# Performance work log

Measured on AMD Instinct MI355X. Metric: run time of the kernel, lower is better.

Reference implementation:

```python
import jax, jax.numpy as jnp
import numpy as np

B, T, V, E, H, DE = 64, 52, 10000, 512, 512, 2048


def _lstm_cell(x, h, c, w_ih, w_hh, b_ih, b_hh):
    # torch.nn.LSTMCell gate order: i, f, g, o
    gates = x @ w_ih.T + h @ w_hh.T + b_ih + b_hh
    i, f, g, o = jnp.split(gates, 4, axis=-1)
    c2 = jax.nn.sigmoid(f) * c + jax.nn.sigmoid(i) * jnp.tanh(g)
    h2 = jax.nn.sigmoid(o) * jnp.tanh(c2)
    return h2, c2


def _run_dir(emb_seq, img, lens, p1, p2, fc_w, fc_b):
    # emb_seq: [B, Td, E]; img: [B, H]; lens: [B] sorted descending.
    # The torch loop slices h[:batch_size_t]; since lens is sorted descending,
    # that is equivalent to masking updates where t >= (len-1). Rows that fall
    # out of the active prefix are never read again, and their predictions stay 0.
    Bd, Td = emb_seq.shape[0], emb_seq.shape[1]
    Hd = img.shape[1]
    mask = jnp.arange(Td)[None, :] < (lens - 1)[:, None]  # [B, Td]
    z = jnp.zeros((Bd, Hd), emb_seq.dtype)

    def step(carry, xs):
        h, c, h1, c1 = carry
        x, m = xs
        m2 = m[:, None]
        hn, cn = _lstm_cell(x, h, c, *p1)
        h1n, c1n = _lstm_cell(jnp.concatenate([hn, img], axis=1), h1, c1, *p2)
        carry = (jnp.where(m2, hn, h), jnp.where(m2, cn, c),
                 jnp.where(m2, h1n, h1), jnp.where(m2, c1n, c1))
        preds = jnp.where(m2, h1n @ fc_w.T + fc_b, 0.0)  # [B, V]
        return carry, preds

    _, preds = jax.lax.scan(step, (z, z, z, z), (emb_seq.transpose(1, 0, 2), mask.T))
    return preds.transpose(1, 0, 2)  # [B, Td, V]


def setup_inputs():
    key = jax.random.key(0)
    ks = iter(jax.random.split(key, 48))

    def u(shape, a=-0.1, b=0.1):
        return jax.random.uniform(next(ks), shape, minval=a, maxval=b, dtype=jnp.float32)

    inp = {}
    inp['encoder_out'] = jax.random.normal(next(ks), (B, DE), dtype=jnp.float32)
    inp['encoded_captions'] = jax.random.randint(next(ks), (B, T), 0, V)
    cl = jax.random.randint(next(ks), (B, 1), 2, T + 1)
    inp['caption_lengths'] = cl.at[0, 0].set(T)  # ensure max decode length = T-1
    # embeddings (uniform -0.1..0.1 per init_weights)
    inp['emb_w'] = u((V, E))
    inp['emb_r_w'] = u((V, E))
    # LSTM cells: torch default init uniform(-1/sqrt(H), 1/sqrt(H))
    kH = 1.0 / np.sqrt(H)
    for name, din in [('1', E), ('2', 2 * H), ('r1', E), ('r2', 2 * H)]:
        inp['w_ih' + name] = u((4 * H, din), -kH, kH)
        inp['w_hh' + name] = u((4 * H, H), -kH, kH)
        inp['b_ih' + name] = u((4 * H,), -kH, kH)
        inp['b_hh' + name] = u((4 * H,), -kH, kH)
    kD = 1.0 / np.sqrt(DE)
    inp['img_f_w'] = u((H, DE), -kD, kD)
    inp['img_f_b'] = u((H,), -kD, kD)
    inp['img_b_w'] = u((H, DE), -kD, kD)
    inp['img_b_b'] = u((H,), -kD, kD)
    inp['fc_w'] = u((V, H))
    inp['fc_b'] = jnp.zeros((V,), jnp.float32)
    inp['fcr_w'] = u((V, H))
    inp['fcr_b'] = jnp.zeros((V,), jnp.float32)
    return inp


def reference(encoder_out, encoded_captions, caption_lengths, emb_w, emb_r_w,
              w_ih1, w_hh1, b_ih1, b_hh1, w_ih2, w_hh2, b_ih2, b_hh2,
              w_ihr1, w_hhr1, b_ihr1, b_hhr1, w_ihr2, w_hhr2, b_ihr2, b_hhr2,
              img_f_w, img_f_b, img_b_w, img_b_b, fc_w, fc_b, fcr_w, fcr_b):
    lens = caption_lengths[:, 0]
    order = jnp.argsort(-lens)  # descending, stable (jax argsort is stable)
    lens = lens[order]
    enc = encoder_out[order]
    caps = encoded_captions[order]
    Tc = caps.shape[1]
    # per-row reversal of the first len tokens; rest zero (matches torch loop)
    j = jnp.arange(Tc)[None, :]
    valid = j < lens[:, None]
    rev_idx = jnp.where(valid, lens[:, None] - 1 - j, 0)
    caps_rev = jnp.where(valid, jnp.take_along_axis(caps, rev_idx, axis=1), 0)
    emb = emb_w[caps]          # [B, T, E]
    emb_r = emb_r_w[caps_rev]  # [B, T, E]
    img_f = enc @ img_f_w.T + img_f_b
    img_r = enc @ img_b_w.T + img_b_b
    Td = Tc - 1  # max(decode_lengths); setup guarantees max(lens) == T
    preds = _run_dir(emb[:, :Td], img_f, lens,
                     (w_ih1, w_hh1, b_ih1, b_hh1), (w_ih2, w_hh2, b_ih2, b_hh2), fc_w, fc_b)
    preds_r = _run_dir(emb_r[:, :Td], img_r, lens,
                       (w_ihr1, w_hhr1, b_ihr1, b_hhr1), (w_ihr2, w_hhr2, b_ihr2, b_hhr2), fcr_w, fcr_b)
    return preds, preds_r, caps, caps_rev, lens - 1, order
```

## Files before the change

kernel.cpp:

```cpp
#include <hip/hip_runtime.h>
#include <stdint.h>

#define B64   64
#define T52   52
#define TD    51
#define V10K  10000
#define MP    3328
#define MR    3264
#define NPFC  10112

typedef float  f32x4  __attribute__((ext_vector_type(4)));
typedef __bf16 bf16x8 __attribute__((ext_vector_type(8)));
typedef unsigned int u32x4 __attribute__((ext_vector_type(4)));
typedef unsigned short ushort_t;

__device__ inline unsigned short f2bf(float f) {
  unsigned u = __builtin_bit_cast(unsigned, f);
  u += 0x7fffu + ((u >> 16) & 1u);
  return (unsigned short)(u >> 16);
}
__device__ inline unsigned pack2(float a, float b) {
  return (unsigned)f2bf(a) | ((unsigned)f2bf(b) << 16);
}
__device__ inline float sigm(float x) { return 1.f / (1.f + expf(-x)); }

__device__ inline void store2_sc(ushort_t* p, unsigned v) {
  asm volatile("global_store_short %0, %1, off sc1" :: "v"(p), "v"(v) : "memory");
}

__global__ void k_prep(const int* __restrict__ cl, const int* __restrict__ caps,
                       float* __restrict__ out_caps, float* __restrict__ out_capr,
                       float* __restrict__ out_lm1, float* __restrict__ out_ord,
                       int* __restrict__ order_i, int* __restrict__ lensm1_i,
                       int* __restrict__ nvtab, int* __restrict__ capsS,
                       int* __restrict__ capsRev)
{
  __shared__ int L[64], O[64], Ls_s[64];
  int i = threadIdx.x;
  L[i] = cl[i];
  __syncthreads();
  if (i == 0) {
    for (int a = 0; a < 64; ++a) O[a] = a;
    for (int a = 1; a < 64; ++a) {
      int key = O[a], kl = L[key], b = a - 1;
      while (b >= 0 && L[O[b]] < kl) { O[b + 1] = O[b]; --b; }
      O[b + 1] = key;
    }
  }
  __syncthreads();
  int src = O[i];
  int Ls  = L[src];
  Ls_s[i] = Ls;
  order_i[i]  = src;
  lensm1_i[i] = Ls - 1;
  out_lm1[i]  = (float)(Ls - 1);
  out_ord[i]  = (float)src;
  int rowLocal[T52];
  for (int t = 0; t < T52; ++t) {
    int c = caps[src * T52 + t];
    rowLocal[t] = c;
    capsS[i * T52 + t]    = c;
    out_caps[i * T52 + t] = (float)c;
  }
  for (int j = 0; j < T52; ++j) {
    int rv = (j < Ls) ? rowLocal[Ls - 1 - j] : 0;
    capsRev[i * T52 + j]  = rv;
    out_capr[i * T52 + j] = (float)rv;
  }
  __syncthreads();
  if (i < TD) {
    int nv = 0;
    for (int r = 0; r < 64; ++r) nv += (Ls_s[r] - 1 > i) ? 1 : 0;
    nvtab[i] = nv;
  }
}

__global__ void k_convert(const float* __restrict__ w_ih1, const float* __restrict__ w_ihr1,
                          const float* __restrict__ fc_w, const float* __restrict__ fcr_w,
                          const float* __restrict__ b_ih1, const float* __restrict__ b_hh1,
                          const float* __restrict__ b_ihr1, const float* __restrict__ b_hhr1,
                          const float* __restrict__ w_hh1, const float* __restrict__ w_hhr1,
                          const float* __restrict__ w_ih2, const float* __restrict__ w_ihr2,
                          const float* __restrict__ w_hh2, const float* __restrict__ w_hhr2,
                          const float* __restrict__ img_f_w, const float* __restrict__ img_b_w,
                          const float* __restrict__ b_ih2, const float* __restrict__ b_hh2,
                          const float* __restrict__ b_ihr2, const float* __restrict__ b_hhr2,
                          const float* __restrict__ enc, const int* __restrict__ order_i,
                          ushort_t* __restrict__ wih1bf, ushort_t* __restrict__ fcwbf,
                          ushort_t* __restrict__ whh1bf, ushort_t* __restrict__ wih2Lbf,
                          ushort_t* __restrict__ whh2bf, ushort_t* __restrict__ wih2Ibf,
                          ushort_t* __restrict__ imgwbf, ushort_t* __restrict__ encbf,
                          float* __restrict__ biasg1, float* __restrict__ biasg2)
{
  long long gid = (long long)blockIdx.x * blockDim.x + threadIdx.x;
  const long long C1 = 2048LL * 512 / 8;
  const long long CF = (long long)NPFC * 512 / 8;
  const long long bs  = 2 * C1 + 2 * CF;
  const long long bs2 = bs + 6 * C1;
  const long long bs3 = bs2 + 2 * C1;
  const long long bs4 = bs3 + 2 * C1;
  const long long bs5 = bs4 + 32768;
  if (gid < 2 * C1) {
    int dir = gid >= C1; long long cid = gid - (long long)dir * C1;
    const float* s = (dir ? w_ihr1 : w_ih1) + cid * 8;
    ushort_t* d = wih1bf + (long long)dir * 2048 * 512 + cid * 8;
    uint4 v;
    v.x = pack2(s[0], s[1]); v.y = pack2(s[2], s[3]);
    v.z = pack2(s[4], s[5]); v.w = pack2(s[6], s[7]);
    *(uint4*)d = v;
  } else if (gid < bs) {
    long long g2 = gid - 2 * C1; int dir = g2 >= CF;
    long long cid = g2 - (long long)dir * CF;
    long long row = cid >> 6; int k8 = (int)(cid & 63) * 8;
    ushort_t* d = fcwbf + (long long)dir * NPFC * 512 + row * 512 + k8;
    uint4 v;
    if (row < V10K) {
      const float* s = (dir ? fcr_w : fc_w) + row * 512 + k8;
      v.x = pack2(s[0], s[1]); v.y = pack2(s[2], s[3]);
      v.z = pack2(s[4], s[5]); v.w = pack2(s[6], s[7]);
    } else { v.x = v.y = v.z = v.w = 0u; }
    *(uint4*)d = v;
  } else if (gid < bs2) {
    long long e = gid - bs;
    int arr = (int)(e / (2 * C1));
    long long d2 = e - (long long)arr * 2 * C1;
    int dir = d2 >= C1;
    long long cid = d2 - (long long)dir * C1;
    long long row = cid >> 6; int k8 = (int)(cid & 63) * 8;
    const float* s;
    ushort_t* d;
    if (arr == 0)      { s = (dir ? w_hhr1 : w_hh1) + row * 512  + k8; d = whh1bf; }
    else if (arr == 1) { s = (dir ? w_ihr2 : w_ih2) + row * 1024 + k8; d = wih2Lbf; }
    else               { s = (dir ? w_hhr2 : w_hh2) + row * 512  + k8; d = whh2bf; }
    d += (long long)dir * 2048 * 512 + cid * 8;
    uint4 v;
    v.x = pack2(s[0], s[1]); v.y = pack2(s[2], s[3]);
    v.z = pack2(s[4], s[5]); v.w = pack2(s[6], s[7]);
    *(uint4*)d = v;
  } else if (gid < bs3) {
    long long e = gid - bs2; int dir = e >= C1;
    long long cid = e - (long long)dir * C1;
    long long row = cid >> 6; int k8 = (int)(cid & 63) * 8;
    const float* s = (dir ? w_ihr2 : w_ih2) + row * 1024 + 512 + k8;
    ushort_t* d = wih2Ibf + (long long)dir * 2048 * 512 + cid * 8;
    uint4 v;
    v.x = pack2(s[0], s[1]); v.y = pack2(s[2], s[3]);
    v.z = pack2(s[4], s[5]); v.w = pack2(s[6], s[7]);
    *(uint4*)d = v;
  } else if (gid < bs4) {
    long long e = gid - bs3; int dir = e >= C1;
    long long cid = e - (long long)dir * C1;
    long long row = cid >> 8; int c8 = (int)(cid & 255) * 8;
    const float* s = (dir ? img_b_w : img_f_w) + row * 2048 + c8;
    ushort_t* d = imgwbf + (long long)dir * 512 * 2048 + cid * 8;
    uint4 v;
    v.x = pack2(s[0], s[1]); v.y = pack2(s[2], s[3]);
    v.z = pack2(s[4], s[5]); v.w = pack2(s[6], s[7]);
    *(uint4*)d = v;
  } else if (gid < bs5) {
    long long cid = gid - bs4;
    int m = (int)(cid >> 8); int c8 = (int)(cid & 255) * 8;
    const float* s = enc + (long long)order_i[m & 63] * 2048 + c8;
    ushort_t* d = encbf + cid * 8;
    uint4 v;
    v.x = pack2(s[0], s[1]); v.y = pack2(s[2], s[3]);
    v.z = pack2(s[4], s[5]); v.w = pack2(s[6], s[7]);
    *(uint4*)d = v;
  } else {
    long long g3 = gid - bs5;
    if (g3 < 4096) {
      int dir = g3 >= 2048; int j = (int)(g3 & 2047);
      biasg1[dir * 2048 + j] = dir ? (b_ihr1[j] + b_hhr1[j]) : (b_ih1[j] + b_hh1[j]);
    } else if (g3 < 8192) {
      long long g4 = g3 - 4096;
      int dir = g4 >= 2048; int j = (int)(g4 & 2047);
      biasg2[dir * 2048 + j] = dir ? (b_ihr2[j] + b_hhr2[j]) : (b_ih2[j] + b_hh2[j]);
    }
  }
}

__global__ void k_gather(const float* __restrict__ emb_w, const float* __restrict__ emb_r_w,
                         const int* __restrict__ capsS, const int* __restrict__ capsRev,
                         ushort_t* __restrict__ embA)
{
  long long gid = (long long)blockIdx.x * 256 + threadIdx.x;
  const long long CPD = (long long)MP * 512 / 8;
  if (gid >= 2 * CPD) return;
  int dir = gid >= CPD; long long cid = gid - (long long)dir * CPD;
  int m = (int)(cid >> 6); int k8 = (int)(cid & 63) * 8;
  ushort_t* d = embA + (long long)dir * MP * 512 + (long long)m * 512 + k8;
  uint4 v;
  if (m < MR) {
    int b = m / TD, t = m - b * TD;
    int row = dir ? capsRev[b * T52 + t] : capsS[b * T52 + t];
    const float* s = (dir ? emb_r_w : emb_w) + (long long)row * 512 + k8;
    v.x = pack2(s[0], s[1]); v.y = pack2(s[2], s[3]);
    v.z = pack2(s[4], s[5]); v.w = pack2(s[6], s[7]);
  } else { v.x = v.y = v.z = v.w = 0u; }
  *(uint4*)d = v;
}

template<int MODE>
__global__ __launch_bounds__(256)
void k_gemm(const ushort_t* __restrict__ A0, long long As,
            const ushort_t* __restrict__ B0, long long Bs,
            const float* __restrict__ bias0, const float* __restrict__ bias1,
            void* __restrict__ out0, long long Os,
            const int* __restrict__ lensm1, int Nreal, int K)
{
  __shared__ ushort_t Ab[128 * 32];
  __shared__ ushort_t Bb[128 * 32];
  int dirz = blockIdx.z;
  const ushort_t* A = A0 + dirz * As;
  const ushort_t* Bm = B0 + dirz * Bs;
  const float* bias = dirz ? bias1 : bias0;
  int tid = threadIdx.x;
  int lane = tid & 63, wid = tid >> 6;
  int wr = wid >> 1, wc = wid & 1;
  long long tm = (long long)blockIdx.x * 128, tn = (long long)blockIdx.y * 128;
  f32x4 acc[4][4] = {};
  int c0 = tid, c1 = tid + 256;
  const ushort_t* Ag0 = A + (tm + (c0 >> 2)) * K + (c0 & 3) * 8;
  const ushort_t* Ag1 = A + (tm + (c1 >> 2)) * K + (c1 & 3) * 8;
  const ushort_t* Bg0 = Bm + (tn + (c0 >> 2)) * K + (c0 & 3) * 8;
  const ushort_t* Bg1 = Bm + (tn + (c1 >> 2)) * K + (c1 & 3) * 8;
  int KK = K >> 5;
  for (int kk = 0; kk < KK; ++kk) {
    uint4 va0 = *(const uint4*)(Ag0 + kk * 32);
    uint4 va1 = *(const uint4*)(Ag1 + kk * 32);
    uint4 vb0 = *(const uint4*)(Bg0 + kk * 32);
    uint4 vb1 = *(const uint4*)(Bg1 + kk * 32);
    __syncthreads();
    *(uint4*)&Ab[c0 * 8] = va0;
    *(uint4*)&Ab[c1 * 8] = va1;
    *(uint4*)&Bb[c0 * 8] = vb0;
    *(uint4*)&Bb[c1 * 8] = vb1;
    __syncthreads();
    int koff = (lane >> 4) * 8;
    bf16x8 av[4], bv[4];
    #pragma unroll
    for (int mi = 0; mi < 4; ++mi)
      av[mi] = *(const bf16x8*)&Ab[(wr * 64 + mi * 16 + (lane & 15)) * 32 + koff];
    #pragma unroll
    for (int ni = 0; ni < 4; ++ni)
      bv[ni] = *(const bf16x8*)&Bb[(wc * 64 + ni * 16 + (lane & 15)) * 32 + koff];
    #pragma unroll
    for (int mi = 0; mi < 4; ++mi)
      #pragma unroll
      for (int ni = 0; ni < 4; ++ni)
        acc[mi][ni] = __builtin_amdgcn_mfma_f32_16x16x32_bf16(av[mi], bv[ni], acc[mi][ni], 0, 0, 0);
  }
  #pragma unroll
  for (int mi = 0; mi < 4; ++mi) {
    #pragma unroll
    for (int rr = 0; rr < 4; ++rr) {
      long long m = tm + wr * 64 + mi * 16 + ((lane >> 4) * 4) + rr;
      if (MODE == 0) {
        float* orow = (float*)out0 + dirz * Os + m * (long long)Nreal;
        #pragma unroll
        for (int ni = 0; ni < 4; ++ni) {
          int n = (int)tn + wc * 64 + ni * 16 + (lane & 15);
          orow[n] = acc[mi][ni][rr] + bias[n];
        }
      } else if (MODE == 1) {
        if (m < MR) {
          int bb = (int)(m / TD); int tt = (int)(m - (long long)bb * TD);
          bool valid = tt < lensm1[bb];
          float* orow = (float*)out0 + dirz * Os + m * (long long)Nreal;
          #pragma unroll
          for (int ni = 0; ni < 4; ++ni) {
            int n = (int)tn + wc * 64 + ni * 16 + (lane & 15);
            if (n < Nreal) orow[n] = valid ? (acc[mi][ni][rr] + bias[n]) : 0.f;
          }
        }
      } else if (MODE == 2) {
        float bm = bias[m];
        float* orow = (float*)out0 + dirz * Os + m * (long long)Nreal;
        #pragma unroll
        for (int ni = 0; ni < 4; ++ni) {
          int n = (int)tn + wc * 64 + ni * 16 + (lane & 15);
          if (n < Nreal) orow[n] = acc[mi][ni][rr] + bm;
        }
      } else {
        ushort_t* orow = (ushort_t*)out0 + dirz * Os + m * (long long)Nreal;
        #pragma unroll
        for (int ni = 0; ni < 4; ++ni) {
          int n = (int)tn + wc * 64 + ni * 16 + (lane & 15);
          orow[n] = f2bf(acc[mi][ni][rr] + bias[n]);
        }
      }
    }
  }
}

__global__ __launch_bounds__(128, 1)
void k_rec(const ushort_t* __restrict__ whh1bf, const ushort_t* __restrict__ wih2Lbf,
           const ushort_t* __restrict__ whh2bf, const float* __restrict__ xg1,
           const float* __restrict__ xg2imgT,
           ushort_t* __restrict__ h1hist,
           ushort_t* __restrict__ h2hist,
           ushort_t* __restrict__ h2allbf, const int* __restrict__ nvtab,
           int* __restrict__ slots)
{
  __builtin_amdgcn_fence(__ATOMIC_ACQUIRE, "agent");
  const int bid = blockIdx.x;
  const int grp = bid & 7;
  const int ht  = bid >> 3;
  const bool isL2 = grp >= 4;
  const int dir  = (grp >> 1) & 1;
  const int half = grp & 1;
  const int tid = threadIdx.x;
  const int lane = tid & 63, mt = tid >> 6;
  const int l15 = lane & 15, l4 = lane >> 4;
  const int jl = ht * 16 + l15;
  const int rbase = half * 32 + mt * 16;
  const int r0 = rbase + l4 * 4;

  __shared__ ushort_t Wl[32768];
  __shared__ ushort_t Wi[32768];
  __shared__ int nv_s[64];

  {
    const ushort_t* src = (isL2 ? whh2bf : whh1bf) + (long long)dir * 2048 * 512;
    #pragma unroll
    for (int i = 0; i < 32; ++i) {
      int c = tid + i * 128;
      int nl = c >> 6;
      int kb = (c & 63) * 16;
      int row = (nl >> 4) * 512 + ht * 16 + (nl & 15);
      u32x4 v = *(const u32x4*)(src + (long long)row * 512 + (long long)(c & 63) * 8);
      *(u32x4*)((char*)Wl + nl * 1024 + (kb ^ ((nl & 7) << 4))) = v;
    }
    if (isL2) {
      const ushort_t* src2 = wih2Lbf + (long long)dir * 2048 * 512;
      #pragma unroll
      for (int i = 0; i < 32; ++i) {
        int c = tid + i * 128;
        int nl = c >> 6;
        int kb = (c & 63) * 16;
        int row = (nl >> 4) * 512 + ht * 16 + (nl & 15);
        u32x4 v = *(const u32x4*)(src2 + (long long)row * 512 + (long long)(c & 63) * 8);
        *(u32x4*)((char*)Wi + nl * 1024 + (kb ^ ((nl & 7) << 4))) = v;
      }
    }
    if (tid < TD) nv_s[tid] = nvtab[tid];
  }
  __syncthreads();

  int* aS = slots + (dir * 2 + half) * 32;
  int* bS = slots + 128 + (dir * 2 + half) * 32;

  if (!isL2) {
    f32x4 creg = {0.f, 0.f, 0.f, 0.f};
    for (int t = 0; t < TD; ++t) {
      bool act = (rbase < nv_s[t]);
      float xs[4][4];
      if (act) {
        #pragma unroll
        for (int g = 0; g < 4; ++g)
          #pragma unroll
          for (int rr = 0; rr < 4; ++rr)
            xs[g][rr] = xg1[((long long)dir * MP + (long long)(r0 + rr) * TD + t) * 2048
                            + g * 512 + jl];
      }
      if (t > 0) {
        if (mt == 0) {
          for (;;) {
            int v = __hip_atomic_load(&aS[lane & 31], __ATOMIC_RELAXED, __HIP_MEMORY_SCOPE_AGENT);
            if (__all(v >= t)) break;
            __builtin_amdgcn_s_sleep(1);
          }
        }
        __syncthreads();
      }
      if (act) {
        const ushort_t* hsrc = h1hist + ((long long)t * 2 + dir) * (64 * 512)
                             + (long long)(rbase + l15) * 512 + l4 * 8;
        u32x4 hv[16];
        #pragma unroll
        for (int kk = 0; kk < 16; ++kk)
          hv[kk] = *(const u32x4*)(hsrc + kk * 32);
        f32x4 acc[4] = {};
        #pragma unroll
        for (int kk = 0; kk < 16; ++kk) {
          bf16x8 av = __builtin_bit_cast(bf16x8, hv[kk]);
          int kb = kk * 64 + l4 * 16;
          #pragma unroll
          for (int g = 0; g < 4; ++g) {
            bf16x8 bv = *(const bf16x8*)((const char*)Wl + (g * 16 + l15) * 1024 + (kb ^ ((l15 & 7) << 4)));
            acc[g] = __builtin_amdgcn_mfma_f32_16x16x32_bf16(av, bv, acc[g], 0, 0, 0);
          }
        }
        ushort_t* hdst = h1hist + ((long long)(t + 1) * 2 + dir) * (64 * 512);
        f32x4 cn;
        #pragma unroll
        for (int rr = 0; rr < 4; ++rr) {
          float gi = acc[0][rr] + xs[0][rr];
          float gf = acc[1][rr] + xs[1][rr];
          float gg = acc[2][rr] + xs[2][rr];
          float go = acc[3][rr] + xs[3][rr];
          float c = sigm(gf) * creg[rr] + sigm(gi) * tanhf(gg);
          float h = sigm(go) * tanhf(c);
          cn[rr] = c;
          store2_sc(hdst + (long long)(r0 + rr) * 512 + jl, (unsigned)f2bf(h));
        }
        creg = cn;
      }
      __syncthreads();
      if (tid == 0)
        __hip_atomic_store(&aS[ht], t + 1, __ATOMIC_RELAXED, __HIP_MEMORY_SCOPE_AGENT);
    }
  } else {
    f32x4 xv2[4];
    {
      const float* xg = xg2imgT + (long long)dir * (2048 * 64);
      #pragma unroll
      for (int g = 0; g < 4; ++g)
        xv2[g] = *(const f32x4*)(xg + (long long)(g * 512 + jl) * 64 + r0);
    }
    f32x4 creg = {0.f, 0.f, 0.f, 0.f};
    for (int t = 0; t < TD; ++t) {
      bool act = (rbase < nv_s[t]);
      int nv = nv_s[t];
      if (mt == 0) {
        for (;;) {
          int v = __hip_atomic_load(&aS[lane & 31], __ATOMIC_RELAXED, __HIP_MEMORY_SCOPE_AGENT);
          if (__all(v >= t + 1)) break;
          __builtin_amdgcn_s_sleep(1);
        }
      }
      __syncthreads();
      f32x4 acc[4] = {};
      if (act) {
        const ushort_t* h1s = h1hist + ((long long)(t + 1) * 2 + dir) * (64 * 512)
                            + (long long)(rbase + l15) * 512 + l4 * 8;
        u32x4 ha[16];
        #pragma unroll
        for (int kk = 0; kk < 16; ++kk) ha[kk] = *(const u32x4*)(h1s + kk * 32);
        #pragma unroll
        for (int kk = 0; kk < 16; ++kk) {
          bf16x8 av = __builtin_bit_cast(bf16x8, ha[kk]);
          int kb = kk * 64 + l4 * 16;
          #pragma unroll
          for (int g = 0; g < 4; ++g) {
            bf16x8 bv = *(const bf16x8*)((const char*)Wi + (g * 16 + l15) * 1024 + (kb ^ ((l15 & 7) << 4)));
            acc[g] = __builtin_amdgcn_mfma_f32_16x16x32_bf16(av, bv, acc[g], 0, 0, 0);
          }
        }
      }
      if (mt == 0) {
        for (;;) {
          int v = __hip_atomic_load(&bS[lane & 31], __ATOMIC_RELAXED, __HIP_MEMORY_SCOPE_AGENT);
          if (__all(v >= t)) break;
          __builtin_amdgcn_s_sleep(1);
        }
      }
      __syncthreads();
      if (act) {
        const ushort_t* h2s = h2hist + ((long long)t * 2 + dir) * (64 * 512)
                            + (long long)(rbase + l15) * 512 + l4 * 8;
        u32x4 hb[16];
        #pragma unroll
        for (int kk = 0; kk < 16; ++kk) hb[kk] = *(const u32x4*)(h2s + kk * 32);
        #pragma unroll
        for (int kk = 0; kk < 16; ++kk) {
          bf16x8 av = __builtin_bit_cast(bf16x8, hb[kk]);
          int kb = kk * 64 + l4 * 16;
          #pragma unroll
          for (int g = 0; g < 4; ++g) {
            bf16x8 bv = *(const bf16x8*)((const char*)Wl + (g * 16 + l15) * 1024 + (kb ^ ((l15 & 7) << 4)));
            acc[g] = __builtin_amdgcn_mfma_f32_16x16x32_bf16(av, bv, acc[g], 0, 0, 0);
          }
        }
        ushort_t* h2n = h2hist + ((long long)(t + 1) * 2 + dir) * (64 * 512);
        ushort_t* h2a = h2allbf + (long long)dir * MP * 512;
        f32x4 cn;
        #pragma unroll
        for (int rr = 0; rr < 4; ++rr) {
          float gi = acc[0][rr] + xv2[0][rr];
          float gf = acc[1][rr] + xv2[1][rr];
          float gg = acc[2][rr] + xv2[2][rr];
          float go = acc[3][rr] + xv2[3][rr];
          float c = sigm(gf) * creg[rr] + sigm(gi) * tanhf(gg);
          float h = sigm(go) * tanhf(c);
          cn[rr] = c;
          ushort_t hbb = f2bf(h);
          store2_sc(h2n + (long long)(r0 + rr) * 512 + jl, (unsigned)hbb);
          if (r0 + rr < nv)
            h2a[((long long)(r0 + rr) * TD + t) * 512 + jl] = hbb;
        }
        creg = cn;
      }
      __syncthreads();
      if (tid == 0)
        __hip_atomic_store(&bS[ht], t + 1, __ATOMIC_RELAXED, __HIP_MEMORY_SCOPE_AGENT);
    }
  }
}

extern "C" void kernel_launch(void* const* d_in, const int* in_sizes, int n_in,
                              void* d_out, int out_size, void* d_ws, size_t ws_size,
                              hipStream_t stream)
{
  const float* enc     = (const float*)d_in[0];
  const int*   caps    = (const int*)d_in[1];
  const int*   cl      = (const int*)d_in[2];
  const float* emb_w   = (const float*)d_in[3];
  const float* emb_r_w = (const float*)d_in[4];
  const float* w_ih1   = (const float*)d_in[5];
  const float* w_hh1   = (const float*)d_in[6];
  const float* b_ih1   = (const float*)d_in[7];
  const float* b_hh1   = (const float*)d_in[8];
  const float* w_ih2   = (const float*)d_in[9];
  const float* w_hh2   = (const float*)d_in[10];
  const float* b_ih2   = (const float*)d_in[11];
  const float* b_hh2   = (const float*)d_in[12];
  const float* w_ihr1  = (const float*)d_in[13];
  const float* w_hhr1  = (const float*)d_in[14];
  const float* b_ihr1  = (const float*)d_in[15];
  const float* b_hhr1  = (const float*)d_in[16];
  const float* w_ihr2  = (const float*)d_in[17];
  const float* w_hhr2  = (const float*)d_in[18];
  const float* b_ihr2  = (const float*)d_in[19];
  const float* b_hhr2  = (const float*)d_in[20];
  const float* img_f_w = (const float*)d_in[21];
  const float* img_f_b = (const float*)d_in[22];
  const float* img_b_w = (const float*)d_in[23];
  const float* img_b_b = (const float*)d_in[24];
  const float* fc_w    = (const float*)d_in[25];
  const float* fc_b    = (const float*)d_in[26];
  const float* fcr_w   = (const float*)d_in[27];
  const float* fcr_b   = (const float*)d_in[28];

  float* outF = (float*)d_out;
  const long long PRED = (long long)MR * V10K;
  float* o_caps = outF + 2 * PRED;
  float* o_capr = o_caps + B64 * T52;
  float* o_lm1  = o_capr + B64 * T52;
  float* o_ord  = o_lm1 + B64;
  float*    xg1       = outF;
  ushort_t* whh1bf    = (ushort_t*)(outF + 27500000);
  ushort_t* wih2Lbf   = (ushort_t*)(outF + 28600000);
  ushort_t* whh2bf    = (ushort_t*)(outF + 29700000);
  ushort_t* h1hist    = (ushort_t*)(outF + 31000000);
  ushort_t* h2hist    = (ushort_t*)(outF + 32800000);
  ushort_t* wih2Ibf   = (ushort_t*)(outF + 34600000);
  ushort_t* imgwbf    = (ushort_t*)(outF + 35700000);
  ushort_t* encbf     = (ushort_t*)(outF + 36800000);
  ushort_t* imgbf     = (ushort_t*)(outF + 37000000);

  char* w = (char*)d_ws;
  auto alloc = [&](size_t bytes) -> char* {
    char* p = w; w += (bytes + 255) & ~(size_t)255; return p;
  };
  int*      order_i  = (int*)alloc(64 * 4);
  int*      lensm1_i = (int*)alloc(64 * 4);
  int*      nvtab    = (int*)alloc(64 * 4);
  int*      capsS    = (int*)alloc(B64 * T52 * 4);
  int*      capsRev  = (int*)alloc(B64 * T52 * 4);
  float*    biasg1   = (float*)alloc(2 * 2048 * 4);
  float*    biasg2   = (float*)alloc(2 * 2048 * 4);
  float*    xg2imgT  = (float*)alloc((size_t)2 * 2048 * 64 * 4);
  int*      slotp    = (int*)alloc(1024);
  ushort_t* embA    = (ushort_t*)alloc((size_t)2 * MP * 512 * 2);
  ushort_t* wih1bf  = (ushort_t*)alloc((size_t)2 * 2048 * 512 * 2);
  ushort_t* fcwbf   = (ushort_t*)alloc((size_t)2 * NPFC * 512 * 2);
  ushort_t* h2allbf = (ushort_t*)alloc((size_t)2 * MP * 512 * 2);

  hipMemsetAsync(slotp, 0, 1024, stream);
  hipMemsetAsync(h1hist, 0, 131072, stream);
  hipMemsetAsync(h2hist, 0, 131072, stream);

  k_prep<<<1, 64, 0, stream>>>(cl, caps, o_caps, o_capr, o_lm1, o_ord,
                               order_i, lensm1_i, nvtab, capsS, capsRev);
  k_convert<<<11360, 256, 0, stream>>>(w_ih1, w_ihr1, fc_w, fcr_w,
                                       b_ih1, b_hh1, b_ihr1, b_hhr1,
                                       w_hh1, w_hhr1, w_ih2, w_ihr2, w_hh2, w_hhr2,
                                       img_f_w, img_b_w, b_ih2, b_hh2, b_ihr2, b_hhr2,
                                       enc, order_i,
                                       wih1bf, fcwbf, whh1bf, wih2Lbf, whh2bf,
                                       wih2Ibf, imgwbf, encbf, biasg1, biasg2);
  k_gather<<<1664, 256, 0, stream>>>(emb_w, emb_r_w, capsS, capsRev, embA);
  k_gemm<3><<<dim3(1, 4, 2), 256, 0, stream>>>(encbf, 0LL,
                                               imgwbf, 512LL * 2048,
                                               img_f_b, img_b_b,
                                               imgbf, 128LL * 512,
                                               nullptr, 512, 2048);
  k_gemm<2><<<dim3(16, 1, 2), 256, 0, stream>>>(wih2Ibf, 2048LL * 512,
                                                imgbf, 128LL * 512,
                                                biasg2, biasg2 + 2048,
                                                xg2imgT, 2048LL * 64,
                                                nullptr, 64, 512);
  k_gemm<0><<<dim3(26, 16, 2), 256, 0, stream>>>(embA, (long long)MP * 512,
                                                 wih1bf, 2048LL * 512,
                                                 biasg1, biasg1 + 2048,
                                                 xg1, (long long)MP * 2048,
                                                 nullptr, 2048, 512);
  k_rec<<<256, 128, 0, stream>>>(whh1bf, wih2Lbf, whh2bf, xg1, xg2imgT,
                                 h1hist, h2hist, h2allbf, nvtab, slotp);
  k_gemm<1><<<dim3(26, 79, 2), 256, 0, stream>>>(h2allbf, (long long)MP * 512,
                                                 fcwbf, (long long)NPFC * 512,
                                                 fc_b, fcr_b,
                                                 outF, PRED,
                                                 lensm1_i, V10K, 512);
}
```

Baseline: 843.5 us.

## Fuse FC projection into persistent recurrence kernel, overlapping output GEMM with time steps

Replaces the recurrence kernel plus the separate vocabulary-projection GEMM with one persistent kernel. 64 blocks run layer 1, 128 blocks run layer 2 with a double-buffered h2 state, and 64 blocks compute the FC output for each time step as soon as that step's h2 is published. The FC blocks also zero the inactive prediction rows while waiting. Input-gate activations for layer 1 are written straight into the predictions buffer and read back from there, and hidden-state loads use batched sc1 inline-asm loads. The goal is to hide the large FC GEMM behind the serial recurrence. The cost is a smaller, less efficient per-step FC tile and more spin-wait synchronisation.

```diff
diff --git a/kernel.cpp b/kernel.cpp
--- a/kernel.cpp
+++ b/kernel.cpp
@@ -26,6 +26,77 @@
 
 __device__ inline void store2_sc(ushort_t* p, unsigned v) {
   asm volatile("global_store_short %0, %1, off sc1" :: "v"(p), "v"(v) : "memory");
+}
+__device__ inline void loadA16(const ushort_t* a, u32x4 (&h)[16]) {
+  asm volatile(
+    "global_load_dwordx4 %0,  %16, off sc1\n\t"
+    "global_load_dwordx4 %1,  %16, off offset:64 sc1\n\t"
+    "global_load_dwordx4 %2,  %16, off offset:128 sc1\n\t"
+    "global_load_dwordx4 %3,  %16, off offset:192 sc1\n\t"
+    "global_load_dwordx4 %4,  %16, off offset:256 sc1\n\t"
+    "global_load_dwordx4 %5,  %16, off offset:320 sc1\n\t"
+    "global_load_dwordx4 %6,  %16, off offset:384 sc1\n\t"
+    "global_load_dwordx4 %7,  %16, off offset:448 sc1\n\t"
+    "global_load_dwordx4 %8,  %16, off offset:512 sc1\n\t"
+    "global_load_dwordx4 %9,  %16, off offset:576 sc1\n\t"
+    "global_load_dwordx4 %10, %16, off offset:640 sc1\n\t"
+    "global_load_dwordx4 %11, %16, off offset:704 sc1\n\t"
+    "global_load_dwordx4 %12, %16, off offset:768 sc1\n\t"
+    "global_load_dwordx4 %13, %16, off offset:832 sc1\n\t"
+    "global_load_dwordx4 %14, %16, off offset:896 sc1\n\t"
+    "global_load_dwordx4 %15, %16, off offset:960 sc1\n\t"
+    "s_waitcnt vmcnt(0)"
+    : "=&v"(h[0]),"=&v"(h[1]),"=&v"(h[2]),"=&v"(h[3]),
+      "=&v"(h[4]),"=&v"(h[5]),"=&v"(h[6]),"=&v"(h[7]),
+      "=&v"(h[8]),"=&v"(h[9]),"=&v"(h[10]),"=&v"(h[11]),
+      "=&v"(h[12]),"=&v"(h[13]),"=&v"(h[14]),"=&v"(h[15])
+    : "v"(a) : "memory");
+}
+__device__ inline void loadA32(const ushort_t* a, const ushort_t* b,
+                               u32x4 (&ha)[16], u32x4 (&hb)[16]) {
+  asm volatile(
+    "global_load_dwordx4 %0,  %32, off sc1\n\t"
+    "global_load_dwordx4 %1,  %32, off offset:64 sc1\n\t"
+    "global_load_dwordx4 %2,  %32, off offset:128 sc1\n\t"
+    "global_load_dwordx4 %3,  %32, off offset:192 sc1\n\t"
+    "global_load_dwordx4 %4,  %32, off offset:256 sc1\n\t"
+    "global_load_dwordx4 %5,  %32, off offset:320 sc1\n\t"
+    "global_load_dwordx4 %6,  %32, off offset:384 sc1\n\t"
+    "global_load_dwordx4 %7,  %32, off offset:448 sc1\n\t"
+    "global_load_dwordx4 %8,  %32, off offset:512 sc1\n\t"
+    "global_load_dwordx4 %9,  %32, off offset:576 sc1\n\t"
+    "global_load_dwordx4 %10, %32, off offset:640 sc1\n\t"
+    "global_load_dwordx4 %11, %32, off offset:704 sc1\n\t"
+    "global_load_dwordx4 %12, %32, off offset:768 sc1\n\t"
+    "global_load_dwordx4 %13, %32, off offset:832 sc1\n\t"
+    "global_load_dwordx4 %14, %32, off offset:896 sc1\n\t"
+    "global_load_dwordx4 %15, %32, off offset:960 sc1\n\t"
+    "global_load_dwordx4 %16, %33, off sc1\n\t"
+    "global_load_dwordx4 %17, %33, off offset:64 sc1\n\t"
+    "global_load_dwordx4 %18, %33, off offset:128 sc1\n\t"
+    "global_load_dwordx4 %19, %33, off offset:192 sc1\n\t"
+    "global_load_dwordx4 %20, %33, off offset:256 sc1\n\t"
+    "global_load_dwordx4 %21, %33, off offset:320 sc1\n\t"
+    "global_load_dwordx4 %22, %33, off offset:384 sc1\n\t"
+    "global_load_dwordx4 %23, %33, off offset:448 sc1\n\t"
+    "global_load_dwordx4 %24, %33, off offset:512 sc1\n\t"
+    "global_load_dwordx4 %25, %33, off offset:576 sc1\n\t"
+    "global_load_dwordx4 %26, %33, off offset:640 sc1\n\t"
+    "global_load_dwordx4 %27, %33, off offset:704 sc1\n\t"
+    "global_load_dwordx4 %28, %33, off offset:768 sc1\n\t"
+    "global_load_dwordx4 %29, %33, off offset:832 sc1\n\t"
+    "global_load_dwordx4 %30, %33, off offset:896 sc1\n\t"
+    "global_load_dwordx4 %31, %33, off offset:960 sc1\n\t"
+    "s_waitcnt vmcnt(0)"
+    : "=&v"(ha[0]),"=&v"(ha[1]),"=&v"(ha[2]),"=&v"(ha[3]),
+      "=&v"(ha[4]),"=&v"(ha[5]),"=&v"(ha[6]),"=&v"(ha[7]),
+      "=&v"(ha[8]),"=&v"(ha[9]),"=&v"(ha[10]),"=&v"(ha[11]),
+      "=&v"(ha[12]),"=&v"(ha[13]),"=&v"(ha[14]),"=&v"(ha[15]),
+      "=&v"(hb[0]),"=&v"(hb[1]),"=&v"(hb[2]),"=&v"(hb[3]),
+      "=&v"(hb[4]),"=&v"(hb[5]),"=&v"(hb[6]),"=&v"(hb[7]),
+      "=&v"(hb[8]),"=&v"(hb[9]),"=&v"(hb[10]),"=&v"(hb[11]),
+      "=&v"(hb[12]),"=&v"(hb[13]),"=&v"(hb[14]),"=&v"(hb[15])
+    : "v"(a), "v"(b) : "memory");
 }
 
 __global__ void k_prep(const int* __restrict__ cl, const int* __restrict__ caps,
@@ -206,7 +277,7 @@
             const ushort_t* __restrict__ B0, long long Bs,
             const float* __restrict__ bias0, const float* __restrict__ bias1,
             void* __restrict__ out0, long long Os,
-            const int* __restrict__ lensm1, int Nreal, int K)
+            int Nreal, int K)
 {
   __shared__ ushort_t Ab[128 * 32];
   __shared__ ushort_t Bb[128 * 32];
@@ -256,21 +327,12 @@
     for (int rr = 0; rr < 4; ++rr) {
       long long m = tm + wr * 64 + mi * 16 + ((lane >> 4) * 4) + rr;
       if (MODE == 0) {
-        float* orow = (float*)out0 + dirz * Os + m * (long long)Nreal;
-        #pragma unroll
-        for (int ni = 0; ni < 4; ++ni) {
-          int n = (int)tn + wc * 64 + ni * 16 + (lane & 15);
-          orow[n] = acc[mi][ni][rr] + bias[n];
-        }
-      } else if (MODE == 1) {
         if (m < MR) {
-          int bb = (int)(m / TD); int tt = (int)(m - (long long)bb * TD);
-          bool valid = tt < lensm1[bb];
           float* orow = (float*)out0 + dirz * Os + m * (long long)Nreal;
           #pragma unroll
           for (int ni = 0; ni < 4; ++ni) {
             int n = (int)tn + wc * 64 + ni * 16 + (lane & 15);
-            if (n < Nreal) orow[n] = valid ? (acc[mi][ni][rr] + bias[n]) : 0.f;
+            orow[n] = acc[mi][ni][rr] + bias[n];
           }
         }
       } else if (MODE == 2) {
@@ -293,75 +355,59 @@
   }
 }
 
-__global__ __launch_bounds__(128, 1)
-void k_rec(const ushort_t* __restrict__ whh1bf, const ushort_t* __restrict__ wih2Lbf,
-           const ushort_t* __restrict__ whh2bf, const float* __restrict__ xg1,
-           const float* __restrict__ xg2imgT,
-           ushort_t* __restrict__ h1hist,
-           ushort_t* __restrict__ h2hist,
-           ushort_t* __restrict__ h2allbf, const int* __restrict__ nvtab,
-           int* __restrict__ slots)
+__global__ __launch_bounds__(256, 1)
+void k_fused(const ushort_t* __restrict__ whh1bf, const ushort_t* __restrict__ wih2Lbf,
+             const ushort_t* __restrict__ whh2bf, float* __restrict__ predsF,
+             const float* __restrict__ xg2imgT,
+             ushort_t* __restrict__ h1hist,
+             ushort_t* __restrict__ h2buf,
+             ushort_t* __restrict__ h2allbf,
+             const ushort_t* __restrict__ fcwbf,
+             const float* __restrict__ fc_b, const float* __restrict__ fcr_b,
+             const int* __restrict__ nvtab, int* __restrict__ slots)
 {
   __builtin_amdgcn_fence(__ATOMIC_ACQUIRE, "agent");
+  const long long PRED = (long long)MR * V10K;
   const int bid = blockIdx.x;
-  const int grp = bid & 7;
-  const int ht  = bid >> 3;
-  const bool isL2 = grp >= 4;
-  const int dir  = (grp >> 1) & 1;
-  const int half = grp & 1;
   const int tid = threadIdx.x;
   const int lane = tid & 63, mt = tid >> 6;
   const int l15 = lane & 15, l4 = lane >> 4;
-  const int jl = ht * 16 + l15;
-  const int rbase = half * 32 + mt * 16;
-  const int r0 = rbase + l4 * 4;
 
   __shared__ ushort_t Wl[32768];
   __shared__ ushort_t Wi[32768];
   __shared__ int nv_s[64];
-
-  {
-    const ushort_t* src = (isL2 ? whh2bf : whh1bf) + (long long)dir * 2048 * 512;
-    #pragma unroll
-    for (int i = 0; i < 32; ++i) {
-      int c = tid + i * 128;
-      int nl = c >> 6;
-      int kb = (c & 63) * 16;
-      int row = (nl >> 4) * 512 + ht * 16 + (nl & 15);
-      u32x4 v = *(const u32x4*)(src + (long long)row * 512 + (long long)(c & 63) * 8);
-      *(u32x4*)((char*)Wl + nl * 1024 + (kb ^ ((nl & 7) << 4))) = v;
-    }
-    if (isL2) {
-      const ushort_t* src2 = wih2Lbf + (long long)dir * 2048 * 512;
+  if (tid < TD) nv_s[tid] = nvtab[tid];
+
+  if (bid < 64) {
+    const int dir = bid >> 5, ht = bid & 31;
+    const int jl = ht * 16 + l15;
+    const int r0 = mt * 16 + l4 * 4;
+    {
+      const ushort_t* src = whh1bf + (long long)dir * 2048 * 512;
       #pragma unroll
-      for (int i = 0; i < 32; ++i) {
-        int c = tid + i * 128;
-        int nl = c >> 6;
-        int kb = (c & 63) * 16;
+      for (int i = 0; i < 16; ++i) {
+        int c = tid + i * 256;
+        int nl = c >> 6, kb = (c & 63) * 16;
         int row = (nl >> 4) * 512 + ht * 16 + (nl & 15);
-        u32x4 v = *(const u32x4*)(src2 + (long long)row * 512 + (long long)(c & 63) * 8);
-        *(u32x4*)((char*)Wi + nl * 1024 + (kb ^ ((nl & 7) << 4))) = v;
-      }
-    }
-    if (tid < TD) nv_s[tid] = nvtab[tid];
-  }
-  __syncthreads();
-
-  int* aS = slots + (dir * 2 + half) * 32;
-  int* bS = slots + 128 + (dir * 2 + half) * 32;
-
-  if (!isL2) {
+        u32x4 v = *(const u32x4*)(src + (long long)row * 512 + (long long)(c & 63) * 8);
+        *(u32x4*)((char*)Wl + nl * 1024 + (kb ^ ((nl & 7) << 4))) = v;
+      }
+    }
+    __syncthreads();
+    int* aS = slots + dir * 32;
+    const float* xb = predsF + (long long)dir * PRED;
     f32x4 creg = {0.f, 0.f, 0.f, 0.f};
     for (int t = 0; t < TD; ++t) {
-      bool act = (rbase < nv_s[t]);
+      bool act = (mt * 16 < nv_s[t]);
       float xs[4][4];
       if (act) {
         #pragma unroll
-        for (int g = 0; g < 4; ++g)
+        for (int rr = 0; rr < 4; ++rr) {
+          long long mrow = (long long)(r0 + rr) * TD + t;
           #pragma unroll
-          for (int rr = 0; rr < 4; ++rr)
-            xs[g][rr] = xg1[((long long)dir * MP + (long long)(r0 + rr) * TD + t) * 2048
-                            + g * 512 + jl];
+          for (int g = 0; g < 4; ++g)
+            xs[g][rr] = xb[mrow * V10K + g * 512 + jl];
+        }
       }
       if (t > 0) {
         if (mt == 0) {
@@ -375,11 +421,9 @@
       }
       if (act) {
         const ushort_t* hsrc = h1hist + ((long long)t * 2 + dir) * (64 * 512)
-                             + (long long)(rbase + l15) * 512 + l4 * 8;
+                             + (long long)(mt * 16 + l15) * 512 + l4 * 8;
         u32x4 hv[16];
-        #pragma unroll
-        for (int kk = 0; kk < 16; ++kk)
-          hv[kk] = *(const u32x4*)(hsrc + kk * 32);
+        loadA16(hsrc, hv);
         f32x4 acc[4] = {};
         #pragma unroll
         for (int kk = 0; kk < 16; ++kk) {
@@ -410,7 +454,34 @@
       if (tid == 0)
         __hip_atomic_store(&aS[ht], t + 1, __ATOMIC_RELAXED, __HIP_MEMORY_SCOPE_AGENT);
     }
-  } else {
+  } else if (bid < 192) {
+    const int idx = bid - 64;
+    const int dir = idx >> 6, sub = idx & 63, half = sub >> 5, ht = sub & 31;
+    const int jl = ht * 16 + l15;
+    const int r0 = half * 32 + (mt & 1) * 16 + l4 * 4;
+    {
+      const ushort_t* src = whh2bf + (long long)dir * 2048 * 512;
+      #pragma unroll
+      for (int i = 0; i < 16; ++i) {
+        int c = tid + i * 256;
+        int nl = c >> 6, kb = (c & 63) * 16;
+        int row = (nl >> 4) * 512 + ht * 16 + (nl & 15);
+        u32x4 v = *(const u32x4*)(src + (long long)row * 512 + (long long)(c & 63) * 8);
+        *(u32x4*)((char*)Wl + nl * 1024 + (kb ^ ((nl & 7) << 4))) = v;
+      }
+      const ushort_t* src2 = wih2Lbf + (long long)dir * 2048 * 512;
+      #pragma unroll
+      for (int i = 0; i < 16; ++i) {
+        int c = tid + i * 256;
+        int nl = c >> 6, kb = (c & 63) * 16;
+        int row = (nl >> 4) * 512 + ht * 16 + (nl & 15);
+        u32x4 v = *(const u32x4*)(src2 + (long long)row * 512 + (long long)(c & 63) * 8);
+        *(u32x4*)((char*)Wi + nl * 1024 + (kb ^ ((nl & 7) << 4))) = v;
+      }
+    }
+    __syncthreads();
+    int* aS = slots + dir * 32;
+    int* bS = slots + 64 + dir * 64;
     f32x4 xv2[4];
     {
       const float* xg = xg2imgT + (long long)dir * (2048 * 64);
@@ -420,23 +491,24 @@
     }
     f32x4 creg = {0.f, 0.f, 0.f, 0.f};
     for (int t = 0; t < TD; ++t) {
-      bool act = (rbase < nv_s[t]);
-      int nv = nv_s[t];
       if (mt == 0) {
         for (;;) {
-          int v = __hip_atomic_load(&aS[lane & 31], __ATOMIC_RELAXED, __HIP_MEMORY_SCOPE_AGENT);
-          if (__all(v >= t + 1)) break;
+          int va = __hip_atomic_load(&aS[lane & 31], __ATOMIC_RELAXED, __HIP_MEMORY_SCOPE_AGENT);
+          int vb = __hip_atomic_load(&bS[lane], __ATOMIC_RELAXED, __HIP_MEMORY_SCOPE_AGENT);
+          if (__all((va >= t + 1) & (vb >= t))) break;
           __builtin_amdgcn_s_sleep(1);
         }
       }
       __syncthreads();
-      f32x4 acc[4] = {};
-      if (act) {
+      int nv = nv_s[t];
+      if (mt < 2 && half * 32 + mt * 16 < nv) {
         const ushort_t* h1s = h1hist + ((long long)(t + 1) * 2 + dir) * (64 * 512)
-                            + (long long)(rbase + l15) * 512 + l4 * 8;
-        u32x4 ha[16];
-        #pragma unroll
-        for (int kk = 0; kk < 16; ++kk) ha[kk] = *(const u32x4*)(h1s + kk * 32);
+                            + (long long)(half * 32 + mt * 16 + l15) * 512 + l4 * 8;
+        const ushort_t* h2s = h2buf + ((long long)((t + 1) & 1) * 2 + dir) * (64 * 512)
+                            + (long long)(half * 32 + mt * 16 + l15) * 512 + l4 * 8;
+        u32x4 ha[16], hb2[16];
+        loadA32(h1s, h2s, ha, hb2);
+        f32x4 acc[4] = {};
         #pragma unroll
         for (int kk = 0; kk < 16; ++kk) {
           bf16x8 av = __builtin_bit_cast(bf16x8, ha[kk]);
@@ -447,24 +519,9 @@
             acc[g] = __builtin_amdgcn_mfma_f32_16x16x32_bf16(av, bv, acc[g], 0, 0, 0);
           }
         }
-      }
-      if (mt == 0) {
-        for (;;) {
-          int v = __hip_atomic_load(&bS[lane & 31], __ATOMIC_RELAXED, __HIP_MEMORY_SCOPE_AGENT);
-          if (__all(v >= t)) break;
-          __builtin_amdgcn_s_sleep(1);
-        }
-      }
-      __syncthreads();
-      if (act) {
-        const ushort_t* h2s = h2hist + ((long long)t * 2 + dir) * (64 * 512)
-                            + (long long)(rbase + l15) * 512 + l4 * 8;
-        u32x4 hb[16];
-        #pragma unroll
-        for (int kk = 0; kk < 16; ++kk) hb[kk] = *(const u32x4*)(h2s + kk * 32);
         #pragma unroll
         for (int kk = 0; kk < 16; ++kk) {
-          bf16x8 av = __builtin_bit_cast(bf16x8, hb[kk]);
+          bf16x8 av = __builtin_bit_cast(bf16x8, hb2[kk]);
           int kb = kk * 64 + l4 * 16;
           #pragma unroll
           for (int g = 0; g < 4; ++g) {
@@ -472,8 +529,8 @@
             acc[g] = __builtin_amdgcn_mfma_f32_16x16x32_bf16(av, bv, acc[g], 0, 0, 0);
           }
         }
-        ushort_t* h2n = h2hist + ((long long)(t + 1) * 2 + dir) * (64 * 512);
-        ushort_t* h2a = h2allbf + (long long)dir * MP * 512;
+        ushort_t* h2n = h2buf + ((long long)(t & 1) * 2 + dir) * (64 * 512);
+        ushort_t* h2a = h2allbf + ((long long)t * 2 + dir) * (64 * 512);
         f32x4 cn;
         #pragma unroll
         for (int rr = 0; rr < 4; ++rr) {
@@ -487,13 +544,87 @@
           ushort_t hbb = f2bf(h);
           store2_sc(h2n + (long long)(r0 + rr) * 512 + jl, (unsigned)hbb);
           if (r0 + rr < nv)
-            h2a[((long long)(r0 + rr) * TD + t) * 512 + jl] = hbb;
+            store2_sc(h2a + (long long)(r0 + rr) * 512 + jl, (unsigned)hbb);
         }
         creg = cn;
       }
       __syncthreads();
       if (tid == 0)
-        __hip_atomic_store(&bS[ht], t + 1, __ATOMIC_RELAXED, __HIP_MEMORY_SCOPE_AGENT);
+        __hip_atomic_store(&bS[half * 32 + ht], t + 1, __ATOMIC_RELAXED, __HIP_MEMORY_SCOPE_AGENT);
+    }
+  } else {
+    const int w = bid - 192;
+    const int dir = w & 1;
+    const int w2 = w >> 1;
+    const ushort_t* fcw = fcwbf + (long long)dir * NPFC * 512;
+    const float* fcb = dir ? fcr_b : fc_b;
+    float* pout = predsF + (long long)dir * PRED;
+    int* bS = slots + 64 + dir * 64;
+    __syncthreads();
+    #pragma unroll 1
+    for (int ti = 0; ti < 3; ++ti) {
+      int vt = w2 + ti * 32; if (vt >= 79) break;
+      int c0 = vt * 128 + lane * 2;
+      #pragma unroll 1
+      for (int t = mt; t < TD; t += 4) {
+        int nv = nv_s[t];
+        #pragma unroll 1
+        for (int b = nv; b < 64; ++b) {
+          long long m = (long long)b * TD + t;
+          if (c0 + 1 < V10K) {
+            float2 z = {0.f, 0.f};
+            *(float2*)(pout + m * V10K + c0) = z;
+          } else if (c0 < V10K) {
+            pout[m * V10K + c0] = 0.f;
+          }
+        }
+      }
+    }
+    for (int t = 0; t < TD; ++t) {
+      if (mt == 0) {
+        for (;;) {
+          int v = __hip_atomic_load(&bS[lane], __ATOMIC_RELAXED, __HIP_MEMORY_SCOPE_AGENT);
+          if (__all(v >= t + 1)) break;
+          __builtin_amdgcn_s_sleep(8);
+        }
+      }
+      __syncthreads();
+      int nv = nv_s[t];
+      const ushort_t* A = h2allbf + ((long long)t * 2 + dir) * (64 * 512);
+      #pragma unroll 1
+      for (int ti = 0; ti < 3; ++ti) {
+        int vt = w2 + ti * 32; if (vt >= 79) break;
+        int base = vt * 128 + mt * 32;
+        f32x4 acc[4][2] = {};
+        #pragma unroll 1
+        for (int kk = 0; kk < 16; ++kk) {
+          int ko = kk * 32 + l4 * 8;
+          bf16x8 bv0 = *(const bf16x8*)(fcw + (long long)(base + l15) * 512 + ko);
+          bf16x8 bv1 = *(const bf16x8*)(fcw + (long long)(base + 16 + l15) * 512 + ko);
+          #pragma unroll
+          for (int mi = 0; mi < 4; ++mi) {
+            bf16x8 av = *(const bf16x8*)(A + (long long)(mi * 16 + l15) * 512 + ko);
+            acc[mi][0] = __builtin_amdgcn_mfma_f32_16x16x32_bf16(av, bv0, acc[mi][0], 0, 0, 0);
+            acc[mi][1] = __builtin_amdgcn_mfma_f32_16x16x32_bf16(av, bv1, acc[mi][1], 0, 0, 0);
+          }
+        }
+        #pragma unroll
+        for (int mi = 0; mi < 4; ++mi) {
+          #pragma unroll
+          for (int rr = 0; rr < 4; ++rr) {
+            int b = mi * 16 + l4 * 4 + rr;
+            if (b < nv) {
+              long long m = (long long)b * TD + t;
+              #pragma unroll
+              for (int ni = 0; ni < 2; ++ni) {
+                int col = base + ni * 16 + l15;
+                if (col < V10K)
+                  pout[m * V10K + col] = acc[mi][ni][rr] + fcb[col];
+              }
+            }
+          }
+        }
+      }
     }
   }
 }
@@ -538,16 +669,6 @@
   float* o_capr = o_caps + B64 * T52;
   float* o_lm1  = o_capr + B64 * T52;
   float* o_ord  = o_lm1 + B64;
-  float*    xg1       = outF;
-  ushort_t* whh1bf    = (ushort_t*)(outF + 27500000);
-  ushort_t* wih2Lbf   = (ushort_t*)(outF + 28600000);
-  ushort_t* whh2bf    = (ushort_t*)(outF + 29700000);
-  ushort_t* h1hist    = (ushort_t*)(outF + 31000000);
-  ushort_t* h2hist    = (ushort_t*)(outF + 32800000);
-  ushort_t* wih2Ibf   = (ushort_t*)(outF + 34600000);
-  ushort_t* imgwbf    = (ushort_t*)(outF + 35700000);
-  ushort_t* encbf     = (ushort_t*)(outF + 36800000);
-  ushort_t* imgbf     = (ushort_t*)(outF + 37000000);
 
   char* w = (char*)d_ws;
   auto alloc = [&](size_t bytes) -> char* {
@@ -562,14 +683,23 @@
   float*    biasg2   = (float*)alloc(2 * 2048 * 4);
   float*    xg2imgT  = (float*)alloc((size_t)2 * 2048 * 64 * 4);
   int*      slotp    = (int*)alloc(1024);
-  ushort_t* embA    = (ushort_t*)alloc((size_t)2 * MP * 512 * 2);
-  ushort_t* wih1bf  = (ushort_t*)alloc((size_t)2 * 2048 * 512 * 2);
-  ushort_t* fcwbf   = (ushort_t*)alloc((size_t)2 * NPFC * 512 * 2);
-  ushort_t* h2allbf = (ushort_t*)alloc((size_t)2 * MP * 512 * 2);
+  ushort_t* embA     = (ushort_t*)alloc((size_t)2 * MP * 512 * 2);
+  ushort_t* wih1bf   = (ushort_t*)alloc((size_t)2 * 2048 * 512 * 2);
+  ushort_t* fcwbf    = (ushort_t*)alloc((size_t)2 * NPFC * 512 * 2);
+  ushort_t* h2allbf  = (ushort_t*)alloc((size_t)TD * 2 * 64 * 512 * 2);
+  ushort_t* whh1bf   = (ushort_t*)alloc((size_t)2 * 2048 * 512 * 2);
+  ushort_t* wih2Lbf  = (ushort_t*)alloc((size_t)2 * 2048 * 512 * 2);
+  ushort_t* whh2bf   = (ushort_t*)alloc((size_t)2 * 2048 * 512 * 2);
+  ushort_t* h1hist   = (ushort_t*)alloc((size_t)T52 * 2 * 64 * 512 * 2);
+  ushort_t* h2buf    = (ushort_t*)alloc((size_t)2 * 2 * 64 * 512 * 2);
+  ushort_t* wih2Ibf  = (ushort_t*)alloc((size_t)2 * 2048 * 512 * 2);
+  ushort_t* imgwbf   = (ushort_t*)alloc((size_t)2 * 512 * 2048 * 2);
+  ushort_t* encbf    = (ushort_t*)alloc((size_t)128 * 2048 * 2);
+  ushort_t* imgbf    = (ushort_t*)alloc((size_t)2 * 128 * 512 * 2);
 
   hipMemsetAsync(slotp, 0, 1024, stream);
   hipMemsetAsync(h1hist, 0, 131072, stream);
-  hipMemsetAsync(h2hist, 0, 131072, stream);
+  hipMemsetAsync(h2buf, 0, 262144, stream);
 
   k_prep<<<1, 64, 0, stream>>>(cl, caps, o_caps, o_capr, o_lm1, o_ord,
                                order_i, lensm1_i, nvtab, capsS, capsRev);
@@ -585,22 +715,18 @@
                                                imgwbf, 512LL * 2048,
                                                img_f_b, img_b_b,
                                                imgbf, 128LL * 512,
-                                               nullptr, 512, 2048);
+                                               512, 2048);
   k_gemm<2><<<dim3(16, 1, 2), 256, 0, stream>>>(wih2Ibf, 2048LL * 512,
                                                 imgbf, 128LL * 512,
                                                 biasg2, biasg2 + 2048,
                                                 xg2imgT, 2048LL * 64,
-                                                nullptr, 64, 512);
+                                                64, 512);
   k_gemm<0><<<dim3(26, 16, 2), 256, 0, stream>>>(embA, (long long)MP * 512,
                                                  wih1bf, 2048LL * 512,
                                                  biasg1, biasg1 + 2048,
-                                                 xg1, (long long)MP * 2048,
-                                                 nullptr, 2048, 512);
-  k_rec<<<256, 128, 0, stream>>>(whh1bf, wih2Lbf, whh2bf, xg1, xg2imgT,
-                                 h1hist, h2hist, h2allbf, nvtab, slotp);
-  k_gemm<1><<<dim3(26, 79, 2), 256, 0, stream>>>(h2allbf, (long long)MP * 512,
-                                                 fcwbf, (long long)NPFC * 512,
-                                                 fc_b, fcr_b,
                                                  outF, PRED,
-                                                 lensm1_i, V10K, 512);
-}
+                                                 V10K, 512);
+  k_fused<<<256, 256, 0, stream>>>(whh1bf, wih2Lbf, whh2bf, outF, xg2imgT,
+                                   h1hist, h2buf, h2allbf, fcwbf,
+                                   fc_b, fcr_b, nvtab, slotp);
+}
```

New measurement: 2.410 ms. +185.7%, slower.
